# Kernel optimization log

Measured on AMD Instinct MI355X. Metric: run time of the kernel, lower is better.

The kernel has to match this reference:

```python
import jax, jax.numpy as jnp
import numpy as np

B, S, D = 8, 1024, 1024
H, K = 16, 64  # num_heads, key_dim
NEG_INF = -1e9  # Keras _large_compatible_negative for float32


def setup_inputs() -> dict:
    key = jax.random.key(0)
    ks = jax.random.split(key, 10)
    x = jax.random.normal(ks[0], (B, S, D), dtype=jnp.float32)
    mask = jax.random.bernoulli(ks[1], 0.9, (B, S))  # bool per-token mask
    w = lambda k, shp: (0.02 * jax.random.normal(k, shp, dtype=jnp.float32))
    return {
        "input_tensor": x,
        "input_mask": mask,
        "Wq": w(ks[2], (D, H, K)), "bq": jnp.zeros((H, K), jnp.float32),
        "Wk": w(ks[3], (D, H, K)), "bk": jnp.zeros((H, K), jnp.float32),
        "Wv": w(ks[4], (D, H, K)), "bv": jnp.zeros((H, K), jnp.float32),
        "Wo": w(ks[5], (H, K, D)), "bo": jnp.zeros((D,), jnp.float32),
    }


def reference(input_tensor, input_mask, Wq, bq, Wk, bk, Wv, bv, Wo, bo):
    x = input_tensor
    # QKV projections: [B,S,D] x [D,H,K] -> [B,S,H,K]
    q = jnp.einsum("bsd,dhk->bshk", x, Wq) + bq
    k = jnp.einsum("bsd,dhk->bshk", x, Wk) + bk
    v = jnp.einsum("bsd,dhk->bshk", x, Wv) + bv
    # scaled dot-product scores: [B,H,Sq,Sk]
    scores = jnp.einsum("bqhk,bshk->bhqs", q, k) / jnp.sqrt(
        jnp.asarray(K, x.dtype))
    # mask = logical_and(mask[...,None], mask[...,None,:]) per example
    m2 = (input_mask[:, :, None] & input_mask[:, None, :])  # [B,Sq,Sk]
    scores = scores + (1.0 - m2[:, None, :, :].astype(x.dtype)) * NEG_INF
    probs = jax.nn.softmax(scores, axis=-1)
    # attend and project out: [B,S,H,K] -> [B,S,D]
    ctx = jnp.einsum("bhqs,bshk->bqhk", probs, v)
    return jnp.einsum("bqhk,hkd->bqd", ctx, Wo) + bo
```

## Files before the change

### kernel.cpp

```cpp
#include <hip/hip_runtime.h>
#include <math.h>

#define Ss 1024
#define Dd 1024
#define Hh 16
#define Kk 64

typedef __bf16 bf16x8 __attribute__((ext_vector_type(8)));
typedef __bf16 bf16x4 __attribute__((ext_vector_type(4)));
typedef float  f32x4  __attribute__((ext_vector_type(4)));

#define MFMA16(a, b, c) __builtin_amdgcn_mfma_f32_16x16x32_bf16(a, b, c, 0, 0, 0)

#define XB_E   8388608u
#define WT_E   3145728u
#define WOT_E  1048576u
#define QKV_E  8388608u

__device__ __forceinline__ float exp2_hw(float x) {
    float r; asm("v_exp_f32 %0, %1" : "=v"(r) : "v"(x)); return r;
}

__global__ __launch_bounds__(256) void prep(
    const float* __restrict__ x,
    const float* __restrict__ Wq, const float* __restrict__ Wk,
    const float* __restrict__ Wv, const float* __restrict__ Wo,
    __bf16* __restrict__ xb, __bf16* __restrict__ WT, __bf16* __restrict__ WoT)
{
    __shared__ float tile[64][65];
    const int z = blockIdx.z;
    const int t = threadIdx.x;

    if (z == 4) {
        size_t blk = blockIdx.y * 16 + blockIdx.x;
        const float4* src = (const float4*)(x + blk * 32768);
        bf16x4* dst = (bf16x4*)(((__bf16*)xb) + blk * 32768);
        #pragma unroll
        for (int u = 0; u < 32; ++u) {
            float4 v = src[u * 256 + t];
            dst[u * 256 + t] =
                (bf16x4){(__bf16)v.x, (__bf16)v.y, (__bf16)v.z, (__bf16)v.w};
        }
        return;
    }

    const float* src = (z == 0) ? Wq : (z == 1) ? Wk : (z == 2) ? Wv : Wo;
    __bf16* dst = (z < 3) ? (WT + (size_t)z * 1048576) : WoT;

    int r0 = blockIdx.y * 64, c0 = blockIdx.x * 64;
    int rr = t >> 2, cg = (t & 3) * 16;

    #pragma unroll
    for (int u = 0; u < 4; ++u) {
        float4 v = *(const float4*)(src + (size_t)(r0 + rr) * 1024 + c0 + cg + u * 4);
        tile[rr][cg + u * 4 + 0] = v.x;
        tile[rr][cg + u * 4 + 1] = v.y;
        tile[rr][cg + u * 4 + 2] = v.z;
        tile[rr][cg + u * 4 + 3] = v.w;
    }
    __syncthreads();
    bf16x8 o0, o1;
    #pragma unroll
    for (int jj = 0; jj < 8; ++jj) o0[jj] = (__bf16)tile[cg + jj][rr];
    #pragma unroll
    for (int jj = 0; jj < 8; ++jj) o1[jj] = (__bf16)tile[cg + 8 + jj][rr];
    __bf16* dp = dst + (size_t)(c0 + rr) * 1024 + r0 + cg;
    *(bf16x8*)dp = o0;
    *(bf16x8*)(dp + 8) = o1;
}

__global__ __launch_bounds__(256) void gemm_bt(
    const __bf16* __restrict__ A, const __bf16* __restrict__ Bt, int mode,
    __bf16* __restrict__ qb, __bf16* __restrict__ kb, __bf16* __restrict__ vb,
    const float* __restrict__ bq, const float* __restrict__ bk,
    const float* __restrict__ bv,
    float* __restrict__ outf, const float* __restrict__ bo)
{
    __shared__ __align__(16) __bf16 As[2][128][32];
    __shared__ __align__(16) __bf16 Bs[2][128][32];

    const int t = threadIdx.x;
    const int wave = t >> 6, lane = t & 63;
    const int quad = lane >> 4, l16 = lane & 15;
    const int wm = wave >> 1, wn = wave & 1;
    const int m0 = blockIdx.y * 128, n0 = blockIdx.x * 128;

    const int sr = t >> 2;
    const int sc = (t & 3) * 8;

    f32x4 acc[4][4];
    #pragma unroll
    for (int i = 0; i < 4; ++i)
        #pragma unroll
        for (int j = 0; j < 4; ++j) acc[i][j] = (f32x4){0.f, 0.f, 0.f, 0.f};

    const __bf16* pa0 = A + (size_t)(m0 + sr) * 1024 + sc;
    const __bf16* pa1 = A + (size_t)(m0 + sr + 64) * 1024 + sc;
    const __bf16* pb0 = Bt + (size_t)(n0 + sr) * 1024 + sc;
    const __bf16* pb1 = Bt + (size_t)(n0 + sr + 64) * 1024 + sc;

    bf16x8 ra0 = *(const bf16x8*)(pa0);
    bf16x8 ra1 = *(const bf16x8*)(pa1);
    bf16x8 rb0 = *(const bf16x8*)(pb0);
    bf16x8 rb1 = *(const bf16x8*)(pb1);

    for (int k0 = 0; k0 < 1024; k0 += 32) {
        const int p = (k0 >> 5) & 1;
        *(bf16x8*)&As[p][sr][sc] = ra0;
        *(bf16x8*)&As[p][sr + 64][sc] = ra1;
        *(bf16x8*)&Bs[p][sr][sc] = rb0;
        *(bf16x8*)&Bs[p][sr + 64][sc] = rb1;
        __syncthreads();

        const int kn = k0 + 32;
        if (kn < 1024) {
            ra0 = *(const bf16x8*)(pa0 + kn);
            ra1 = *(const bf16x8*)(pa1 + kn);
            rb0 = *(const bf16x8*)(pb0 + kn);
            rb1 = *(const bf16x8*)(pb1 + kn);
        }

        bf16x8 af[4], bfr[4];
        #pragma unroll
        for (int i = 0; i < 4; ++i)
            af[i] = *(const bf16x8*)&As[p][wm * 64 + i * 16 + l16][quad * 8];
        #pragma unroll
        for (int j = 0; j < 4; ++j)
            bfr[j] = *(const bf16x8*)&Bs[p][wn * 64 + j * 16 + l16][quad * 8];
        #pragma unroll
        for (int i = 0; i < 4; ++i)
            #pragma unroll
            for (int j = 0; j < 4; ++j)
                acc[i][j] = MFMA16(af[i], bfr[j], acc[i][j]);
    }

    if (mode == 0) {
        const int z = n0 >> 10;
        const float* bias = (z == 0) ? bq : (z == 1) ? bk : bv;
        const float sc2 = (z == 0) ? 0.18033688011112042f : 1.0f;
        #pragma unroll
        for (int i = 0; i < 4; ++i) {
            int row = m0 + wm * 64 + i * 16 + quad * 4;
            int b = row >> 10, s = row & 1023;
            #pragma unroll
            for (int j = 0; j < 4; ++j) {
                int n1 = (n0 + wn * 64 + j * 16 + l16) & 1023;
                int h = n1 >> 6, ch = n1 & 63;
                float bia = bias[n1];
                if (z < 2) {
                    __bf16* dst = ((z == 0) ? qb : kb)
                        + ((size_t)(b * Hh + h) * Ss + s) * Kk + ch;
                    #pragma unroll
                    for (int r = 0; r < 4; ++r)
                        dst[(size_t)r * Kk] = (__bf16)((acc[i][j][r] + bia) * sc2);
                } else {
                    bf16x4 o;
                    #pragma unroll
                    for (int r = 0; r < 4; ++r) o[r] = (__bf16)(acc[i][j][r] + bia);
                    *(bf16x4*)(vb + ((size_t)(b * Hh + h) * Kk + ch) * Ss + s) = o;
                }
            }
        }
    } else {
        #pragma unroll
        for (int i = 0; i < 4; ++i) {
            int row = m0 + wm * 64 + i * 16 + quad * 4;
            #pragma unroll
            for (int j = 0; j < 4; ++j) {
                int n = n0 + wn * 64 + j * 16 + l16;
                float bia = bo[n];
                #pragma unroll
                for (int r = 0; r < 4; ++r)
                    outf[(size_t)(row + r) * 1024 + n] = acc[i][j][r] + bia;
            }
        }
    }
}

__global__ __launch_bounds__(256) void attn(
    const __bf16* __restrict__ qb, const __bf16* __restrict__ kb,
    const __bf16* __restrict__ vb, const int* __restrict__ mask,
    __bf16* __restrict__ ctx)
{
    const int bh = blockIdx.x;
    const int q0 = blockIdx.y * 128;
    const int b  = bh >> 4;
    const int h  = bh & 15;
    const size_t base = (size_t)bh * Ss * Kk;

    __shared__ __align__(16) __bf16 Qs[128][72];
    __shared__ __align__(16) __bf16 Ks[2][64][72];
    __shared__ __align__(16) __bf16 VTs[2][64][72];
    __shared__ __align__(16) __bf16 Ps[4][32][72];
    __shared__ float mkf[1024];

    const int t    = threadIdx.x;
    const int wave = t >> 6, lane = t & 63;
    const int quad = lane >> 4, l16 = lane & 15;
    const int qbase = wave * 32;

    #pragma unroll
    for (int p = 0; p < 4; ++p) {
        int idx = t + p * 256;
        int r = idx >> 3, g = idx & 7;
        *(bf16x8*)&Qs[r][g * 8] =
            *(const bf16x8*)(qb + base + (size_t)(q0 + r) * Kk + g * 8);
    }
    {
        int4 mi = *(const int4*)(mask + b * Ss + t * 4);
        mkf[t * 4 + 0] = (float)mi.x;
        mkf[t * 4 + 1] = (float)mi.y;
        mkf[t * 4 + 2] = (float)mi.z;
        mkf[t * 4 + 3] = (float)mi.w;
    }

    const int r0 = t >> 3, c0 = (t & 7) * 8;
    bf16x8 kr0, kr1, vr0, vr1;
    kr0 = *(const bf16x8*)(kb + base + (size_t)(r0) * Kk + c0);
    kr1 = *(const bf16x8*)(kb + base + (size_t)(r0 + 32) * Kk + c0);
    vr0 = *(const bf16x8*)(vb + base + (size_t)(r0) * Ss + c0);
    vr1 = *(const bf16x8*)(vb + base + (size_t)(r0 + 32) * Ss + c0);

    __syncthreads();

    bf16x8 aq[2][2];
    #pragma unroll
    for (int rg = 0; rg < 2; ++rg) {
        aq[rg][0] = *(const bf16x8*)&Qs[qbase + rg * 16 + l16][quad * 8];
        aq[rg][1] = *(const bf16x8*)&Qs[qbase + rg * 16 + l16][32 + quad * 8];
    }
    float mqf[2][4], omqf[2][4];
    #pragma unroll
    for (int rg = 0; rg < 2; ++rg)
        #pragma unroll
        for (int i = 0; i < 4; ++i) {
            float m = mkf[q0 + qbase + rg * 16 + quad * 4 + i];
            mqf[rg][i] = m; omqf[rg][i] = 1.0f - m;
        }

    f32x4 O[2][4];
    float lsum[2][4];
    #pragma unroll
    for (int rg = 0; rg < 2; ++rg)
        #pragma unroll
        for (int nb = 0; nb < 4; ++nb) O[rg][nb] = (f32x4){0.f, 0.f, 0.f, 0.f};
    #pragma unroll
    for (int rg = 0; rg < 2; ++rg)
        #pragma unroll
        for (int i = 0; i < 4; ++i) lsum[rg][i] = 0.f;

    for (int kt = 0; kt < Ss; kt += 64) {
        const int p = (kt >> 6) & 1;
        *(bf16x8*)&Ks[p][r0][c0] = kr0;
        *(bf16x8*)&Ks[p][r0 + 32][c0] = kr1;
        *(bf16x8*)&VTs[p][r0][c0] = vr0;
        *(bf16x8*)&VTs[p][r0 + 32][c0] = vr1;
        __syncthreads();

        int ktn = kt + 64;
        if (ktn < Ss) {
            kr0 = *(const bf16x8*)(kb + base + (size_t)(ktn + r0) * Kk + c0);
            kr1 = *(const bf16x8*)(kb + base + (size_t)(ktn + r0 + 32) * Kk + c0);
            vr0 = *(const bf16x8*)(vb + base + (size_t)(r0) * Ss + ktn + c0);
            vr1 = *(const bf16x8*)(vb + base + (size_t)(r0 + 32) * Ss + ktn + c0);
        }

        float mkv[4];
        #pragma unroll
        for (int nb = 0; nb < 4; ++nb) mkv[nb] = mkf[kt + nb * 16 + l16];

        bf16x8 kb0[4], kb1[4];
        #pragma unroll
        for (int nb = 0; nb < 4; ++nb) {
            kb0[nb] = *(const bf16x8*)&Ks[p][nb * 16 + l16][quad * 8];
            kb1[nb] = *(const bf16x8*)&Ks[p][nb * 16 + l16][32 + quad * 8];
        }

        f32x4 s[2][4];
        __builtin_amdgcn_s_setprio(1);
        #pragma unroll
        for (int rg = 0; rg < 2; ++rg)
            #pragma unroll
            for (int nb = 0; nb < 4; ++nb) {
                f32x4 a = (f32x4){0.f, 0.f, 0.f, 0.f};
                a = MFMA16(aq[rg][0], kb0[nb], a);
                a = MFMA16(aq[rg][1], kb1[nb], a);
                s[rg][nb] = a;
            }
        __builtin_amdgcn_s_setprio(0);

        #pragma unroll
        for (int rg = 0; rg < 2; ++rg)
            #pragma unroll
            for (int i = 0; i < 4; ++i) {
                float ls = 0.f;
                #pragma unroll
                for (int nb = 0; nb < 4; ++nb) {
                    float pv = exp2_hw(s[rg][nb][i]) * mkv[nb];
                    pv = pv * mqf[rg][i] + omqf[rg][i];
                    Ps[wave][rg * 16 + quad * 4 + i][nb * 16 + l16] = (__bf16)pv;
                    ls += pv;
                }
                lsum[rg][i] += ls;
            }

        bf16x8 ap0[2], ap1[2];
        #pragma unroll
        for (int rg = 0; rg < 2; ++rg) {
            ap0[rg] = *(const bf16x8*)&Ps[wave][rg * 16 + l16][quad * 8];
            ap1[rg] = *(const bf16x8*)&Ps[wave][rg * 16 + l16][32 + quad * 8];
        }
        __builtin_amdgcn_s_setprio(1);
        #pragma unroll
        for (int nb = 0; nb < 4; ++nb) {
            bf16x8 vb0 = *(const bf16x8*)&VTs[p][nb * 16 + l16][quad * 8];
            bf16x8 vb1 = *(const bf16x8*)&VTs[p][nb * 16 + l16][32 + quad * 8];
            #pragma unroll
            for (int rg = 0; rg < 2; ++rg) {
                O[rg][nb] = MFMA16(ap0[rg], vb0, O[rg][nb]);
                O[rg][nb] = MFMA16(ap1[rg], vb1, O[rg][nb]);
            }
        }
        __builtin_amdgcn_s_setprio(0);
    }

    #pragma unroll
    for (int rg = 0; rg < 2; ++rg)
        #pragma unroll
        for (int i = 0; i < 4; ++i) {
            float l = lsum[rg][i];
            l += __shfl_xor(l, 1);
            l += __shfl_xor(l, 2);
            l += __shfl_xor(l, 4);
            l += __shfl_xor(l, 8);
            float inv = 1.0f / l;
            int srow = q0 + qbase + rg * 16 + quad * 4 + i;
            __bf16* dst = ctx + ((size_t)(b * Ss + srow) * Hh + h) * Kk;
            #pragma unroll
            for (int nb = 0; nb < 4; ++nb)
                dst[nb * 16 + l16] = (__bf16)(O[rg][nb][i] * inv);
        }
}

extern "C" void kernel_launch(void* const* d_in, const int* in_sizes, int n_in,
                              void* d_out, int out_size, void* d_ws, size_t ws_size,
                              hipStream_t stream) {
    const float* x    = (const float*)d_in[0];
    const int*   mask = (const int*)d_in[1];
    const float* Wq   = (const float*)d_in[2];
    const float* bq   = (const float*)d_in[3];
    const float* Wk   = (const float*)d_in[4];
    const float* bk   = (const float*)d_in[5];
    const float* Wv   = (const float*)d_in[6];
    const float* bv   = (const float*)d_in[7];
    const float* Wo   = (const float*)d_in[8];
    const float* bo   = (const float*)d_in[9];

    __bf16* xb   = (__bf16*)d_ws;
    __bf16* WT   = xb + XB_E;
    __bf16* WoT  = WT + WT_E;
    __bf16* qb   = WoT + WOT_E;
    __bf16* kb   = qb + QKV_E;
    __bf16* vb   = kb + QKV_E;
    __bf16* ctxb = vb + QKV_E;
    float* out = (float*)d_out;

    prep<<<dim3(16, 16, 5), 256, 0, stream>>>(x, Wq, Wk, Wv, Wo, xb, WT, WoT);
    gemm_bt<<<dim3(24, 64), 256, 0, stream>>>(xb, WT, 0, qb, kb, vb,
                                              bq, bk, bv, nullptr, nullptr);
    attn<<<dim3(128, 8), 256, 0, stream>>>(qb, kb, vb, mask, ctxb);
    gemm_bt<<<dim3(8, 64), 256, 0, stream>>>(ctxb, WoT, 1, nullptr, nullptr,
                                             nullptr, nullptr, nullptr, nullptr,
                                             out, bo);
}
```

Before: 271.7 us.

## Rewrite GEMM with direct global-to-LDS loads, swizzled LDS, larger tiles

The projection GEMM now uses 512-thread blocks on 256x128 output tiles with a K-step of 64. Operands are loaded straight into shared memory with global_load_lds, and the LDS layout is XOR-swizzled to avoid bank conflicts. Loads are double-buffered with explicit vmcnt waits and barriers, and MFMA sections are raised in priority with s_setprio. This removes the register staging and LDS store instructions and gives more MFMA work per K-step. In exchange it uses more LDS per block and fewer blocks, and its correctness depends on hand-placed waitcnt and barrier ordering.

```diff
diff --git a/kernel.cpp b/kernel.cpp
--- a/kernel.cpp
+++ b/kernel.cpp
@@ -19,6 +19,12 @@
 
 __device__ __forceinline__ float exp2_hw(float x) {
     float r; asm("v_exp_f32 %0, %1" : "=v"(r) : "v"(x)); return r;
+}
+
+typedef __attribute__((address_space(1))) const void gas_void;
+typedef __attribute__((address_space(3))) void las_void;
+__device__ __forceinline__ void gll16(const __bf16* g, char* l) {
+    __builtin_amdgcn_global_load_lds((gas_void*)g, (las_void*)l, 16, 0, 0);
 }
 
 __global__ __launch_bounds__(256) void prep(
@@ -69,24 +75,40 @@
     *(bf16x8*)(dp + 8) = o1;
 }
 
-__global__ __launch_bounds__(256) void gemm_bt(
+__global__ __launch_bounds__(512, 2) void gemm_bt(
     const __bf16* __restrict__ A, const __bf16* __restrict__ Bt, int mode,
     __bf16* __restrict__ qb, __bf16* __restrict__ kb, __bf16* __restrict__ vb,
     const float* __restrict__ bq, const float* __restrict__ bk,
     const float* __restrict__ bv,
     float* __restrict__ outf, const float* __restrict__ bo)
 {
-    __shared__ __align__(16) __bf16 As[2][128][32];
-    __shared__ __align__(16) __bf16 Bs[2][128][32];
+    __shared__ __align__(16) __bf16 As[2][256][64];
+    __shared__ __align__(16) __bf16 Bs[2][128][64];
 
     const int t = threadIdx.x;
     const int wave = t >> 6, lane = t & 63;
     const int quad = lane >> 4, l16 = lane & 15;
     const int wm = wave >> 1, wn = wave & 1;
-    const int m0 = blockIdx.y * 128, n0 = blockIdx.x * 128;
-
-    const int sr = t >> 2;
-    const int sc = (t & 3) * 8;
+    const int m0 = blockIdx.y * 256, n0 = blockIdx.x * 128;
+
+    const int srow = t >> 3;
+    const int scol = (((t & 7) ^ ((t >> 3) & 7)) * 8);
+    const __bf16* pa = A  + (size_t)(m0 + srow) * 1024 + scol;
+    const __bf16* pb = Bt + (size_t)(n0 + srow) * 1024 + scol;
+    char* lA = (char*)(&As[0][0][0]) + t * 16;
+    char* lB = (char*)(&Bs[0][0][0]) + t * 16;
+
+#define STAGE(slot, k0) do {                                   \
+        gll16(pa + (k0),           lA + (slot) * 32768);       \
+        gll16(pa + (k0) +  65536,  lA + (slot) * 32768 +  8192); \
+        gll16(pa + (k0) + 131072,  lA + (slot) * 32768 + 16384); \
+        gll16(pa + (k0) + 196608,  lA + (slot) * 32768 + 24576); \
+        gll16(pb + (k0),           lB + (slot) * 16384);       \
+        gll16(pb + (k0) +  65536,  lB + (slot) * 16384 +  8192); \
+    } while (0)
+
+    STAGE(0, 0);
+    STAGE(1, 64);
 
     f32x4 acc[4][4];
     #pragma unroll
@@ -94,84 +116,104 @@
         #pragma unroll
         for (int j = 0; j < 4; ++j) acc[i][j] = (f32x4){0.f, 0.f, 0.f, 0.f};
 
-    const __bf16* pa0 = A + (size_t)(m0 + sr) * 1024 + sc;
-    const __bf16* pa1 = A + (size_t)(m0 + sr + 64) * 1024 + sc;
-    const __bf16* pb0 = Bt + (size_t)(n0 + sr) * 1024 + sc;
-    const __bf16* pb1 = Bt + (size_t)(n0 + sr + 64) * 1024 + sc;
-
-    bf16x8 ra0 = *(const bf16x8*)(pa0);
-    bf16x8 ra1 = *(const bf16x8*)(pa1);
-    bf16x8 rb0 = *(const bf16x8*)(pb0);
-    bf16x8 rb1 = *(const bf16x8*)(pb1);
-
-    for (int k0 = 0; k0 < 1024; k0 += 32) {
-        const int p = (k0 >> 5) & 1;
-        *(bf16x8*)&As[p][sr][sc] = ra0;
-        *(bf16x8*)&As[p][sr + 64][sc] = ra1;
-        *(bf16x8*)&Bs[p][sr][sc] = rb0;
-        *(bf16x8*)&Bs[p][sr + 64][sc] = rb1;
-        __syncthreads();
-
-        const int kn = k0 + 32;
-        if (kn < 1024) {
-            ra0 = *(const bf16x8*)(pa0 + kn);
-            ra1 = *(const bf16x8*)(pa1 + kn);
-            rb0 = *(const bf16x8*)(pb0 + kn);
-            rb1 = *(const bf16x8*)(pb1 + kn);
-        }
-
-        bf16x8 af[4], bfr[4];
-        #pragma unroll
-        for (int i = 0; i < 4; ++i)
-            af[i] = *(const bf16x8*)&As[p][wm * 64 + i * 16 + l16][quad * 8];
-        #pragma unroll
-        for (int j = 0; j < 4; ++j)
-            bfr[j] = *(const bf16x8*)&Bs[p][wn * 64 + j * 16 + l16][quad * 8];
-        #pragma unroll
-        for (int i = 0; i < 4; ++i)
-            #pragma unroll
-            for (int j = 0; j < 4; ++j)
-                acc[i][j] = MFMA16(af[i], bfr[j], acc[i][j]);
-    }
+    const int swz = (l16 & 7) << 4;
+
+    for (int it = 0; it < 16; ++it) {
+        const int s = it & 1;
+        if (it == 0) asm volatile("s_waitcnt vmcnt(6)" ::: "memory");
+        else         asm volatile("s_waitcnt vmcnt(0)" ::: "memory");
+        __builtin_amdgcn_s_barrier();
+
+        if (it >= 1 && it < 15) STAGE(s ^ 1, (it + 1) * 64);
+
+        const char* baseA = (const char*)&As[s][0][0];
+        const char* baseB = (const char*)&Bs[s][0][0];
+
+        bf16x8 bfrag[2][4];
+        #pragma unroll
+        for (int nj = 0; nj < 4; ++nj) {
+            int rowb = (wn * 64 + nj * 16 + l16) * 128;
+            bfrag[0][nj] = *(const bf16x8*)(baseB + rowb + ((quad * 16) ^ swz));
+            bfrag[1][nj] = *(const bf16x8*)(baseB + rowb + ((64 + quad * 16) ^ swz));
+        }
+
+        {
+            bf16x8 afr[2][2];
+            #pragma unroll
+            for (int mi = 0; mi < 2; ++mi) {
+                int rowa = (wm * 64 + mi * 16 + l16) * 128;
+                afr[mi][0] = *(const bf16x8*)(baseA + rowa + ((quad * 16) ^ swz));
+                afr[mi][1] = *(const bf16x8*)(baseA + rowa + ((64 + quad * 16) ^ swz));
+            }
+            __builtin_amdgcn_s_setprio(1);
+            #pragma unroll
+            for (int mi = 0; mi < 2; ++mi)
+                #pragma unroll
+                for (int nj = 0; nj < 4; ++nj)
+                    acc[mi][nj] = MFMA16(afr[mi][1], bfrag[1][nj],
+                                  MFMA16(afr[mi][0], bfrag[0][nj], acc[mi][nj]));
+            __builtin_amdgcn_s_setprio(0);
+        }
+        __builtin_amdgcn_s_barrier();
+
+        {
+            bf16x8 afr[2][2];
+            #pragma unroll
+            for (int mi = 0; mi < 2; ++mi) {
+                int rowa = (wm * 64 + (mi + 2) * 16 + l16) * 128;
+                afr[mi][0] = *(const bf16x8*)(baseA + rowa + ((quad * 16) ^ swz));
+                afr[mi][1] = *(const bf16x8*)(baseA + rowa + ((64 + quad * 16) ^ swz));
+            }
+            __builtin_amdgcn_s_setprio(1);
+            #pragma unroll
+            for (int mi = 0; mi < 2; ++mi)
+                #pragma unroll
+                for (int nj = 0; nj < 4; ++nj)
+                    acc[mi + 2][nj] = MFMA16(afr[mi][1], bfrag[1][nj],
+                                      MFMA16(afr[mi][0], bfrag[0][nj], acc[mi + 2][nj]));
+            __builtin_amdgcn_s_setprio(0);
+        }
+    }
+#undef STAGE
 
     if (mode == 0) {
         const int z = n0 >> 10;
         const float* bias = (z == 0) ? bq : (z == 1) ? bk : bv;
         const float sc2 = (z == 0) ? 0.18033688011112042f : 1.0f;
         #pragma unroll
-        for (int i = 0; i < 4; ++i) {
-            int row = m0 + wm * 64 + i * 16 + quad * 4;
-            int b = row >> 10, s = row & 1023;
-            #pragma unroll
-            for (int j = 0; j < 4; ++j) {
-                int n1 = (n0 + wn * 64 + j * 16 + l16) & 1023;
+        for (int mi = 0; mi < 4; ++mi) {
+            int row = m0 + wm * 64 + mi * 16 + quad * 4;
+            int b = row >> 10, sx = row & 1023;
+            #pragma unroll
+            for (int nj = 0; nj < 4; ++nj) {
+                int n1 = (n0 + wn * 64 + nj * 16 + l16) & 1023;
                 int h = n1 >> 6, ch = n1 & 63;
                 float bia = bias[n1];
                 if (z < 2) {
                     __bf16* dst = ((z == 0) ? qb : kb)
-                        + ((size_t)(b * Hh + h) * Ss + s) * Kk + ch;
+                        + ((size_t)(b * Hh + h) * Ss + sx) * Kk + ch;
                     #pragma unroll
                     for (int r = 0; r < 4; ++r)
-                        dst[(size_t)r * Kk] = (__bf16)((acc[i][j][r] + bia) * sc2);
+                        dst[(size_t)r * Kk] = (__bf16)((acc[mi][nj][r] + bia) * sc2);
                 } else {
                     bf16x4 o;
                     #pragma unroll
-                    for (int r = 0; r < 4; ++r) o[r] = (__bf16)(acc[i][j][r] + bia);
-                    *(bf16x4*)(vb + ((size_t)(b * Hh + h) * Kk + ch) * Ss + s) = o;
+                    for (int r = 0; r < 4; ++r) o[r] = (__bf16)(acc[mi][nj][r] + bia);
+                    *(bf16x4*)(vb + ((size_t)(b * Hh + h) * Kk + ch) * Ss + sx) = o;
                 }
             }
         }
     } else {
         #pragma unroll
-        for (int i = 0; i < 4; ++i) {
-            int row = m0 + wm * 64 + i * 16 + quad * 4;
-            #pragma unroll
-            for (int j = 0; j < 4; ++j) {
-                int n = n0 + wn * 64 + j * 16 + l16;
+        for (int mi = 0; mi < 4; ++mi) {
+            int row = m0 + wm * 64 + mi * 16 + quad * 4;
+            #pragma unroll
+            for (int nj = 0; nj < 4; ++nj) {
+                int n = n0 + wn * 64 + nj * 16 + l16;
                 float bia = bo[n];
                 #pragma unroll
                 for (int r = 0; r < 4; ++r)
-                    outf[(size_t)(row + r) * 1024 + n] = acc[i][j][r] + bia;
+                    outf[(size_t)(row + r) * 1024 + n] = acc[mi][nj][r] + bia;
             }
         }
     }
@@ -366,10 +408,10 @@
     float* out = (float*)d_out;
 
     prep<<<dim3(16, 16, 5), 256, 0, stream>>>(x, Wq, Wk, Wv, Wo, xb, WT, WoT);
-    gemm_bt<<<dim3(24, 64), 256, 0, stream>>>(xb, WT, 0, qb, kb, vb,
+    gemm_bt<<<dim3(24, 32), 512, 0, stream>>>(xb, WT, 0, qb, kb, vb,
                                               bq, bk, bv, nullptr, nullptr);
     attn<<<dim3(128, 8), 256, 0, stream>>>(qb, kb, vb, mask, ctxb);
-    gemm_bt<<<dim3(8, 64), 256, 0, stream>>>(ctxb, WoT, 1, nullptr, nullptr,
+    gemm_bt<<<dim3(8, 32), 512, 0, stream>>>(ctxb, WoT, 1, nullptr, nullptr,
                                              nullptr, nullptr, nullptr, nullptr,
                                              out, bo);
 }
```

Result: slower. 279.3 us (+2.8%).
